# Kernel tuning notes

Hardware: AMD Instinct MI355X
Metric: run time of the kernel (lower is better)

Reference implementation:

```python
import jax, jax.numpy as jnp
import numpy as np

TOKENS = 1024
IN_W = 512
BLOCK = 256
OUT_W = 512
N_BLOCKS = 64
K = 2


def setup_inputs() -> dict:
    key = jax.random.key(0)
    ks = jax.random.split(key, 8)
    u = lambda k, s: jax.random.uniform(k, s, jnp.float32, -1.0, 1.0)
    return {
        "x": jax.random.normal(ks[0], (TOKENS, IN_W), jnp.float32),
        "noise": jax.random.normal(ks[1], (TOKENS, N_BLOCKS), jnp.float32),
        "w1s": u(ks[2], (N_BLOCKS, IN_W, BLOCK)),
        "b1s": u(ks[3], (N_BLOCKS, BLOCK)),
        "w2s": u(ks[4], (N_BLOCKS, BLOCK, OUT_W)),
        "b2s": u(ks[5], (N_BLOCKS, OUT_W)),
        "mixer": jnp.zeros((IN_W, N_BLOCKS), jnp.float32) + 0.01 * jax.random.normal(ks[6], (IN_W, N_BLOCKS), jnp.float32),
        "noise_controller": jnp.zeros((IN_W, N_BLOCKS), jnp.float32) + 0.01 * jax.random.normal(ks[7], (IN_W, N_BLOCKS), jnp.float32),
        "k": K,
    }


def reference(x, noise, w1s, b1s, w2s, b2s, mixer, noise_controller, k):
    # noisy routing logits: mixer_prod + randn * softplus(noise_prod)
    h_x = x @ mixer + noise * jax.nn.softplus(x @ noise_controller)  # [B, E]
    topk_vals, topk_idx = jax.lax.top_k(h_x, k)                       # [B, K]
    scores = jax.nn.softmax(topk_vals, axis=-1)                       # [B, K]
    # per-token expert weight gather (faithful to index_select semantics)
    gw1 = w1s[topk_idx]  # [B, K, I, H]
    gb1 = b1s[topk_idx]  # [B, K, H]
    gw2 = w2s[topk_idx]  # [B, K, H, O]
    gb2 = b2s[topk_idx]  # [B, K, O]
    v = jax.nn.relu(jnp.einsum('bi,bkih->bkh', x, gw1) + gb1)        # [B, K, H]
    out = jnp.einsum('bkh,bkho->bko', v, gw2) + gb2                   # [B, K, O]
    return jnp.sum(out * scores[..., None], axis=1)                   # [B, O]
```

## Files before the change

### kernel.cpp

```cpp
#include <hip/hip_runtime.h>
#include <math.h>

#define TOKENS    1024
#define IN_W      512
#define BLOCK_H   256
#define OUT_W     512
#define N_EXPERTS 64
#define TOPK      2
#define NSLOTS    (TOKENS * TOPK)
#define LIST_CAP  128
#define T_GRP     12
#define NGRP      4
#define XPAD      520
#define OSPAD     516
#define VPAD      264

__global__ __launch_bounds__(256) void routing_kernel(
    const float* __restrict__ x, const float* __restrict__ noise,
    const float* __restrict__ mixer, const float* __restrict__ noisec,
    float* __restrict__ esc, int* __restrict__ counts, int* __restrict__ lists)
{
    __shared__ float xs[2 * 512];
    __shared__ float pm[2 * 2 * 64];
    __shared__ float pn[2 * 2 * 64];
    const int blk  = blockIdx.x;
    const int tid  = threadIdx.x;
    const int wave = tid >> 6, lane = tid & 63;
    const int tq = wave >> 1;
    const int ih = wave & 1;

    ((float4*)xs)[tid] = ((const float4*)x)[(size_t)blk * 256 + tid];
    __syncthreads();

    float am = 0.f, an = 0.f;
    const float* xp = xs + tq * 512 + ih * 256;
    const float* mp = mixer  + (size_t)(ih * 256) * 64 + lane;
    const float* np = noisec + (size_t)(ih * 256) * 64 + lane;
    #pragma unroll 8
    for (int i = 0; i < 256; ++i) {
        const float xv = xp[i];
        am = fmaf(xv, mp[i * 64], am);
        an = fmaf(xv, np[i * 64], an);
    }
    pm[tq * 128 + ih * 64 + lane] = am;
    pn[tq * 128 + ih * 64 + lane] = an;
    __syncthreads();

    if (tid < 128) {
        const int e = tid & 63, tt = tid >> 6;
        const int t = blk * 2 + tt;
        const float am2 = pm[tt * 128 + e] + pm[tt * 128 + 64 + e];
        const float an2 = pn[tt * 128 + e] + pn[tt * 128 + 64 + e];
        const float sp = fmaxf(an2, 0.f) + log1pf(expf(-fabsf(an2)));
        pm[tt * 128 + e] = am2 + noise[(size_t)t * 64 + e] * sp;
    }
    __syncthreads();

    if (tid < 2) {
        const float* h = pm + tid * 128;
        float b0 = -INFINITY, b1 = -INFINITY;
        int i0 = 0, i1 = 0;
        for (int i = 0; i < N_EXPERTS; ++i) {
            const float v = h[i];
            if (v > b0)      { b1 = b0; i1 = i0; b0 = v; i0 = i; }
            else if (v > b1) { b1 = v; i1 = i; }
        }
        const float z   = expf(b1 - b0);
        const float inv = 1.f / (1.f + z);
        const int t = blk * 2 + tid;
        esc[t * 2 + 0] = inv;
        esc[t * 2 + 1] = z * inv;
        const int p0 = atomicAdd(&counts[i0], 1);
        if (p0 < LIST_CAP) lists[i0 * LIST_CAP + p0] = t * 2 + 0;
        const int p1 = atomicAdd(&counts[i1], 1);
        if (p1 < LIST_CAP) lists[i1 * LIST_CAP + p1] = t * 2 + 1;
    }
}

__global__ __launch_bounds__(1024, 4) void expert_kernel(
    const float* __restrict__ x,
    const float* __restrict__ w1s, const float* __restrict__ b1s,
    const float* __restrict__ w2s, const float* __restrict__ b2s,
    const int* __restrict__ counts, const int* __restrict__ lists,
    const float* __restrict__ esc, float* __restrict__ out)
{
    __shared__ __align__(16) float smem[T_GRP * XPAD];
    __shared__ __align__(16) float vsm[T_GRP * VPAD];
    __shared__ int   slotIds[T_GRP];
    __shared__ float escv[T_GRP];

    const int e  = blockIdx.x;
    const int g  = blockIdx.y;
    const int ne = min(counts[e], LIST_CAP);
    const int tid  = threadIdx.x;
    const int wave = tid >> 6, lane = tid & 63;

    const int c4 = lane & 15;
    const int r4 = (lane >> 4) << 2;
    const int cq1   = wave & 3;
    const int t0_1  = (wave >> 2) * 3;
    const int wcol1 = cq1 * 16 + c4;
    const int co2   = wave & 7;
    const int t0_2  = (wave >> 3) * 6;
    const int wcol2 = co2 * 16 + c4;

    const float4* w1v = (const float4*)(w1s + (size_t)e * IN_W * BLOCK_H);
    const float4* w2v = (const float4*)(w2s + (size_t)e * BLOCK_H * OUT_W);
    const float4* b1v = (const float4*)(b1s + (size_t)e * BLOCK_H);
    const float4* b2v = (const float4*)(b2s + (size_t)e * OUT_W);
    const float4* x4  = (const float4*)x;

    for (int base = g * T_GRP; base < ne; base += NGRP * T_GRP) {
        const int nTok = min(T_GRP, ne - base);
        if (tid < T_GRP) {
            const int s = (tid < nTok) ? lists[e * LIST_CAP + base + tid] : 0;
            slotIds[tid] = s;
            escv[tid]    = esc[s];
        }
        __syncthreads();

        for (int idx = tid; idx < T_GRP * 128; idx += 1024) {
            const int t = idx >> 7, q = idx & 127;
            float4 v = make_float4(0.f, 0.f, 0.f, 0.f);
            if (t < nTok) v = x4[(size_t)(slotIds[t] >> 1) * 128 + q];
            *(float4*)&smem[t * XPAD + q * 4] = v;
        }
        __syncthreads();

        {
            float4 a0 = make_float4(0.f,0.f,0.f,0.f), a1 = a0, a2 = a0;
            const float4* wp  = w1v + (size_t)r4 * 64 + wcol1;
            const float*  xr0 = smem + (t0_1 + 0) * XPAD + r4;
            const float*  xr1 = smem + (t0_1 + 1) * XPAD + r4;
            const float*  xr2 = smem + (t0_1 + 2) * XPAD + r4;
            float4 wb[4], wc[4];
            #pragma unroll
            for (int k = 0; k < 4; ++k) wb[k] = wp[(size_t)k * 64];
            for (int i = 0; i < IN_W; i += 16) {
                #pragma unroll
                for (int k = 0; k < 4; ++k) wc[k] = wb[k];
                if (i + 16 < IN_W) {
                    #pragma unroll
                    for (int k = 0; k < 4; ++k)
                        wb[k] = wp[(size_t)(i + 16 + k) * 64];
                }
                const float4 xv0 = *(const float4*)(xr0 + i);
                const float4 xv1 = *(const float4*)(xr1 + i);
                const float4 xv2 = *(const float4*)(xr2 + i);
                const float* f0 = (const float*)&xv0;
                const float* f1 = (const float*)&xv1;
                const float* f2 = (const float*)&xv2;
                #pragma unroll
                for (int k = 0; k < 4; ++k) {
                    const float4 w = wc[k];
                    a0.x = fmaf(f0[k], w.x, a0.x); a0.y = fmaf(f0[k], w.y, a0.y);
                    a0.z = fmaf(f0[k], w.z, a0.z); a0.w = fmaf(f0[k], w.w, a0.w);
                    a1.x = fmaf(f1[k], w.x, a1.x); a1.y = fmaf(f1[k], w.y, a1.y);
                    a1.z = fmaf(f1[k], w.z, a1.z); a1.w = fmaf(f1[k], w.w, a1.w);
                    a2.x = fmaf(f2[k], w.x, a2.x); a2.y = fmaf(f2[k], w.y, a2.y);
                    a2.z = fmaf(f2[k], w.z, a2.z); a2.w = fmaf(f2[k], w.w, a2.w);
                }
            }
            #pragma unroll
            for (int m = 16; m <= 32; m <<= 1) {
                a0.x += __shfl_xor(a0.x, m); a0.y += __shfl_xor(a0.y, m);
                a0.z += __shfl_xor(a0.z, m); a0.w += __shfl_xor(a0.w, m);
                a1.x += __shfl_xor(a1.x, m); a1.y += __shfl_xor(a1.y, m);
                a1.z += __shfl_xor(a1.z, m); a1.w += __shfl_xor(a1.w, m);
                a2.x += __shfl_xor(a2.x, m); a2.y += __shfl_xor(a2.y, m);
                a2.z += __shfl_xor(a2.z, m); a2.w += __shfl_xor(a2.w, m);
            }
            if (lane < 16) {
                const float4 bb = b1v[wcol1];
                float4 r;
                r.x = fmaxf(a0.x + bb.x, 0.f); r.y = fmaxf(a0.y + bb.y, 0.f);
                r.z = fmaxf(a0.z + bb.z, 0.f); r.w = fmaxf(a0.w + bb.w, 0.f);
                *(float4*)&vsm[(t0_1 + 0) * VPAD + wcol1 * 4] = r;
                r.x = fmaxf(a1.x + bb.x, 0.f); r.y = fmaxf(a1.y + bb.y, 0.f);
                r.z = fmaxf(a1.z + bb.z, 0.f); r.w = fmaxf(a1.w + bb.w, 0.f);
                *(float4*)&vsm[(t0_1 + 1) * VPAD + wcol1 * 4] = r;
                r.x = fmaxf(a2.x + bb.x, 0.f); r.y = fmaxf(a2.y + bb.y, 0.f);
                r.z = fmaxf(a2.z + bb.z, 0.f); r.w = fmaxf(a2.w + bb.w, 0.f);
                *(float4*)&vsm[(t0_1 + 2) * VPAD + wcol1 * 4] = r;
            }
        }
        __syncthreads();

        {
            float4 acc[6];
            #pragma unroll
            for (int j = 0; j < 6; ++j) acc[j] = make_float4(0.f,0.f,0.f,0.f);
            const float4* wp2 = w2v + (size_t)r4 * 128 + wcol2;
            const float*  vr  = vsm + t0_2 * VPAD + r4;
            float4 wb[4], wc[4];
            #pragma unroll
            for (int k = 0; k < 4; ++k) wb[k] = wp2[(size_t)k * 128];
            for (int h = 0; h < BLOCK_H; h += 16) {
                #pragma unroll
                for (int k = 0; k < 4; ++k) wc[k] = wb[k];
                if (h + 16 < BLOCK_H) {
                    #pragma unroll
                    for (int k = 0; k < 4; ++k)
                        wb[k] = wp2[(size_t)(h + 16 + k) * 128];
                }
                float4 vv[6];
                #pragma unroll
                for (int j = 0; j < 6; ++j)
                    vv[j] = *(const float4*)(vr + j * VPAD + h);
                #pragma unroll
                for (int k = 0; k < 4; ++k) {
                    const float4 w = wc[k];
                    #pragma unroll
                    for (int j = 0; j < 6; ++j) {
                        const float s = ((const float*)&vv[j])[k];
                        acc[j].x = fmaf(s, w.x, acc[j].x);
                        acc[j].y = fmaf(s, w.y, acc[j].y);
                        acc[j].z = fmaf(s, w.z, acc[j].z);
                        acc[j].w = fmaf(s, w.w, acc[j].w);
                    }
                }
            }
            #pragma unroll
            for (int m = 16; m <= 32; m <<= 1) {
                #pragma unroll
                for (int j = 0; j < 6; ++j) {
                    acc[j].x += __shfl_xor(acc[j].x, m);
                    acc[j].y += __shfl_xor(acc[j].y, m);
                    acc[j].z += __shfl_xor(acc[j].z, m);
                    acc[j].w += __shfl_xor(acc[j].w, m);
                }
            }
            if (lane < 16) {
                #pragma unroll
                for (int j = 0; j < 6; ++j)
                    *(float4*)&smem[(t0_2 + j) * OSPAD + wcol2 * 4] = acc[j];
            }
        }
        __syncthreads();

        for (int idx = tid; idx < T_GRP * 128; idx += 1024) {
            const int t = idx >> 7, q = idx & 127;
            if (t < nTok) {
                const float4 r  = *(const float4*)&smem[t * OSPAD + q * 4];
                const float4 bb = b2v[q];
                const float  sc = escv[t];
                float* o = out + (size_t)(slotIds[t] >> 1) * OUT_W + q * 4;
                atomicAdd(o + 0, (r.x + bb.x) * sc);
                atomicAdd(o + 1, (r.y + bb.y) * sc);
                atomicAdd(o + 2, (r.z + bb.z) * sc);
                atomicAdd(o + 3, (r.w + bb.w) * sc);
            }
        }
        __syncthreads();
    }
}

extern "C" void kernel_launch(void* const* d_in, const int* in_sizes, int n_in,
                              void* d_out, int out_size, void* d_ws, size_t ws_size,
                              hipStream_t stream) {
    const float* x      = (const float*)d_in[0];
    const float* noise  = (const float*)d_in[1];
    const float* w1s    = (const float*)d_in[2];
    const float* b1s    = (const float*)d_in[3];
    const float* w2s    = (const float*)d_in[4];
    const float* b2s    = (const float*)d_in[5];
    const float* mixer  = (const float*)d_in[6];
    const float* noisec = (const float*)d_in[7];
    float* out = (float*)d_out;

    char* ws = (char*)d_ws;
    int*   counts = (int*)ws;                       ws += 256;
    float* esc    = (float*)ws;                     ws += NSLOTS * sizeof(float);
    int*   lists  = (int*)ws;

    hipMemsetAsync(d_out, 0, (size_t)out_size * sizeof(float), stream);
    hipMemsetAsync(counts, 0, 256, stream);

    routing_kernel<<<TOKENS / 2, 256, 0, stream>>>(x, noise, mixer, noisec,
                                                   esc, counts, lists);
    expert_kernel<<<dim3(N_EXPERTS, NGRP), 1024, 0, stream>>>(
        x, w1s, b1s, w2s, b2s, counts, lists, esc, out);
}
```

Baseline: 185.0 us.

## Split expert GEMM reduction across waves so each weight is loaded once

Both expert matmuls are remapped so every wave covers all 12 tokens of the group for a slice of the reduction dimension. Stage 1 uses a 4-way K split and stage 2 a 2-way K split, instead of splitting tokens across waves. Before, each weight element was fetched by several waves, one per token subset. Now it is fetched once per block and reused across all tokens held in registers. Partial sums go through a new shared-memory buffer and are combined by an extra reduction pass and barrier. This costs more LDS (lower occupancy) and more accumulator registers.

Result: slower. 298.4 us (+61.3%).

```diff
diff --git a/kernel.cpp b/kernel.cpp
--- a/kernel.cpp
+++ b/kernel.cpp
@@ -12,8 +12,13 @@
 #define T_GRP     12
 #define NGRP      4
 #define XPAD      520
-#define OSPAD     516
-#define VPAD      264
+#define VPAD      260
+#define P2PAD     516
+
+__device__ __forceinline__ void fma4(float4& a, float s, const float4& w) {
+    a.x = fmaf(s, w.x, a.x); a.y = fmaf(s, w.y, a.y);
+    a.z = fmaf(s, w.z, a.z); a.w = fmaf(s, w.w, a.w);
+}
 
 __global__ __launch_bounds__(256) void routing_kernel(
     const float* __restrict__ x, const float* __restrict__ noise,
@@ -84,8 +89,9 @@
     const int* __restrict__ counts, const int* __restrict__ lists,
     const float* __restrict__ esc, float* __restrict__ out)
 {
-    __shared__ __align__(16) float smem[T_GRP * XPAD];
+    __shared__ __align__(16) float xs[T_GRP * XPAD];
     __shared__ __align__(16) float vsm[T_GRP * VPAD];
+    __shared__ __align__(16) float psum[4 * T_GRP * VPAD];
     __shared__ int   slotIds[T_GRP];
     __shared__ float escv[T_GRP];
 
@@ -94,15 +100,15 @@
     const int ne = min(counts[e], LIST_CAP);
     const int tid  = threadIdx.x;
     const int wave = tid >> 6, lane = tid & 63;
-
     const int c4 = lane & 15;
-    const int r4 = (lane >> 4) << 2;
-    const int cq1   = wave & 3;
-    const int t0_1  = (wave >> 2) * 3;
-    const int wcol1 = cq1 * 16 + c4;
-    const int co2   = wave & 7;
-    const int t0_2  = (wave >> 3) * 6;
-    const int wcol2 = co2 * 16 + c4;
+    const int rg = lane >> 4;
+
+    const int cq   = wave & 3,  kq = wave >> 2;
+    const int col1 = cq * 16 + c4;
+    const int k1   = kq * 128 + rg * 4;
+    const int oct  = wave & 7,  kh = wave >> 3;
+    const int col2 = oct * 16 + c4;
+    const int k2   = kh * 128 + rg * 4;
 
     const float4* w1v = (const float4*)(w1s + (size_t)e * IN_W * BLOCK_H);
     const float4* w2v = (const float4*)(w2s + (size_t)e * BLOCK_H * OUT_W);
@@ -123,117 +129,110 @@
             const int t = idx >> 7, q = idx & 127;
             float4 v = make_float4(0.f, 0.f, 0.f, 0.f);
             if (t < nTok) v = x4[(size_t)(slotIds[t] >> 1) * 128 + q];
-            *(float4*)&smem[t * XPAD + q * 4] = v;
+            *(float4*)&xs[t * XPAD + q * 4] = v;
         }
         __syncthreads();
 
         {
-            float4 a0 = make_float4(0.f,0.f,0.f,0.f), a1 = a0, a2 = a0;
-            const float4* wp  = w1v + (size_t)r4 * 64 + wcol1;
-            const float*  xr0 = smem + (t0_1 + 0) * XPAD + r4;
-            const float*  xr1 = smem + (t0_1 + 1) * XPAD + r4;
-            const float*  xr2 = smem + (t0_1 + 2) * XPAD + r4;
-            float4 wb[4], wc[4];
+            float4 acc[T_GRP];
+            #pragma unroll
+            for (int t = 0; t < T_GRP; ++t) acc[t] = make_float4(0.f,0.f,0.f,0.f);
+            const float4* wp = w1v + (size_t)k1 * 64 + col1;
+            float4 wb[4];
             #pragma unroll
             for (int k = 0; k < 4; ++k) wb[k] = wp[(size_t)k * 64];
-            for (int i = 0; i < IN_W; i += 16) {
+            for (int i = 0; i < 128; i += 16) {
+                float4 wc[4];
                 #pragma unroll
                 for (int k = 0; k < 4; ++k) wc[k] = wb[k];
-                if (i + 16 < IN_W) {
+                if (i + 16 < 128) {
                     #pragma unroll
                     for (int k = 0; k < 4; ++k)
                         wb[k] = wp[(size_t)(i + 16 + k) * 64];
                 }
-                const float4 xv0 = *(const float4*)(xr0 + i);
-                const float4 xv1 = *(const float4*)(xr1 + i);
-                const float4 xv2 = *(const float4*)(xr2 + i);
-                const float* f0 = (const float*)&xv0;
-                const float* f1 = (const float*)&xv1;
-                const float* f2 = (const float*)&xv2;
-                #pragma unroll
-                for (int k = 0; k < 4; ++k) {
-                    const float4 w = wc[k];
-                    a0.x = fmaf(f0[k], w.x, a0.x); a0.y = fmaf(f0[k], w.y, a0.y);
-                    a0.z = fmaf(f0[k], w.z, a0.z); a0.w = fmaf(f0[k], w.w, a0.w);
-                    a1.x = fmaf(f1[k], w.x, a1.x); a1.y = fmaf(f1[k], w.y, a1.y);
-                    a1.z = fmaf(f1[k], w.z, a1.z); a1.w = fmaf(f1[k], w.w, a1.w);
-                    a2.x = fmaf(f2[k], w.x, a2.x); a2.y = fmaf(f2[k], w.y, a2.y);
-                    a2.z = fmaf(f2[k], w.z, a2.z); a2.w = fmaf(f2[k], w.w, a2.w);
+                #pragma unroll
+                for (int t = 0; t < T_GRP; ++t) {
+                    const float4 xv = *(const float4*)&xs[t * XPAD + k1 + i];
+                    fma4(acc[t], xv.x, wc[0]);
+                    fma4(acc[t], xv.y, wc[1]);
+                    fma4(acc[t], xv.z, wc[2]);
+                    fma4(acc[t], xv.w, wc[3]);
                 }
             }
             #pragma unroll
             for (int m = 16; m <= 32; m <<= 1) {
-                a0.x += __shfl_xor(a0.x, m); a0.y += __shfl_xor(a0.y, m);
-                a0.z += __shfl_xor(a0.z, m); a0.w += __shfl_xor(a0.w, m);
-                a1.x += __shfl_xor(a1.x, m); a1.y += __shfl_xor(a1.y, m);
-                a1.z += __shfl_xor(a1.z, m); a1.w += __shfl_xor(a1.w, m);
-                a2.x += __shfl_xor(a2.x, m); a2.y += __shfl_xor(a2.y, m);
-                a2.z += __shfl_xor(a2.z, m); a2.w += __shfl_xor(a2.w, m);
+                #pragma unroll
+                for (int t = 0; t < T_GRP; ++t) {
+                    acc[t].x += __shfl_xor(acc[t].x, m);
+                    acc[t].y += __shfl_xor(acc[t].y, m);
+                    acc[t].z += __shfl_xor(acc[t].z, m);
+                    acc[t].w += __shfl_xor(acc[t].w, m);
+                }
             }
             if (lane < 16) {
-                const float4 bb = b1v[wcol1];
-                float4 r;
-                r.x = fmaxf(a0.x + bb.x, 0.f); r.y = fmaxf(a0.y + bb.y, 0.f);
-                r.z = fmaxf(a0.z + bb.z, 0.f); r.w = fmaxf(a0.w + bb.w, 0.f);
-                *(float4*)&vsm[(t0_1 + 0) * VPAD + wcol1 * 4] = r;
-                r.x = fmaxf(a1.x + bb.x, 0.f); r.y = fmaxf(a1.y + bb.y, 0.f);
-                r.z = fmaxf(a1.z + bb.z, 0.f); r.w = fmaxf(a1.w + bb.w, 0.f);
-                *(float4*)&vsm[(t0_1 + 1) * VPAD + wcol1 * 4] = r;
-                r.x = fmaxf(a2.x + bb.x, 0.f); r.y = fmaxf(a2.y + bb.y, 0.f);
-                r.z = fmaxf(a2.z + bb.z, 0.f); r.w = fmaxf(a2.w + bb.w, 0.f);
-                *(float4*)&vsm[(t0_1 + 2) * VPAD + wcol1 * 4] = r;
-            }
+                #pragma unroll
+                for (int t = 0; t < T_GRP; ++t)
+                    *(float4*)&psum[(kq * T_GRP + t) * VPAD + col1 * 4] = acc[t];
+            }
+        }
+        __syncthreads();
+
+        if (tid < T_GRP * 64) {
+            const int t = tid >> 6, c = tid & 63;
+            const float4 s0 = *(const float4*)&psum[(0 * T_GRP + t) * VPAD + c * 4];
+            const float4 s1 = *(const float4*)&psum[(1 * T_GRP + t) * VPAD + c * 4];
+            const float4 s2 = *(const float4*)&psum[(2 * T_GRP + t) * VPAD + c * 4];
+            const float4 s3 = *(const float4*)&psum[(3 * T_GRP + t) * VPAD + c * 4];
+            const float4 bb = b1v[c];
+            float4 r;
+            r.x = fmaxf(s0.x + s1.x + s2.x + s3.x + bb.x, 0.f);
+            r.y = fmaxf(s0.y + s1.y + s2.y + s3.y + bb.y, 0.f);
+            r.z = fmaxf(s0.z + s1.z + s2.z + s3.z + bb.z, 0.f);
+            r.w = fmaxf(s0.w + s1.w + s2.w + s3.w + bb.w, 0.f);
+            *(float4*)&vsm[t * VPAD + c * 4] = r;
         }
         __syncthreads();
 
         {
-            float4 acc[6];
-            #pragma unroll
-            for (int j = 0; j < 6; ++j) acc[j] = make_float4(0.f,0.f,0.f,0.f);
-            const float4* wp2 = w2v + (size_t)r4 * 128 + wcol2;
-            const float*  vr  = vsm + t0_2 * VPAD + r4;
-            float4 wb[4], wc[4];
+            float4 acc[T_GRP];
+            #pragma unroll
+            for (int t = 0; t < T_GRP; ++t) acc[t] = make_float4(0.f,0.f,0.f,0.f);
+            const float4* wp2 = w2v + (size_t)k2 * 128 + col2;
+            float4 wb[4];
             #pragma unroll
             for (int k = 0; k < 4; ++k) wb[k] = wp2[(size_t)k * 128];
-            for (int h = 0; h < BLOCK_H; h += 16) {
+            for (int i = 0; i < 128; i += 16) {
+                float4 wc[4];
                 #pragma unroll
                 for (int k = 0; k < 4; ++k) wc[k] = wb[k];
-                if (h + 16 < BLOCK_H) {
+                if (i + 16 < 128) {
                     #pragma unroll
                     for (int k = 0; k < 4; ++k)
-                        wb[k] = wp2[(size_t)(h + 16 + k) * 128];
-                }
-                float4 vv[6];
-                #pragma unroll
-                for (int j = 0; j < 6; ++j)
-                    vv[j] = *(const float4*)(vr + j * VPAD + h);
-                #pragma unroll
-                for (int k = 0; k < 4; ++k) {
-                    const float4 w = wc[k];
-                    #pragma unroll
-                    for (int j = 0; j < 6; ++j) {
-                        const float s = ((const float*)&vv[j])[k];
-                        acc[j].x = fmaf(s, w.x, acc[j].x);
-                        acc[j].y = fmaf(s, w.y, acc[j].y);
-                        acc[j].z = fmaf(s, w.z, acc[j].z);
-                        acc[j].w = fmaf(s, w.w, acc[j].w);
-                    }
+                        wb[k] = wp2[(size_t)(i + 16 + k) * 128];
+                }
+                #pragma unroll
+                for (int t = 0; t < T_GRP; ++t) {
+                    const float4 vv = *(const float4*)&vsm[t * VPAD + k2 + i];
+                    fma4(acc[t], vv.x, wc[0]);
+                    fma4(acc[t], vv.y, wc[1]);
+                    fma4(acc[t], vv.z, wc[2]);
+                    fma4(acc[t], vv.w, wc[3]);
                 }
             }
             #pragma unroll
             for (int m = 16; m <= 32; m <<= 1) {
                 #pragma unroll
-                for (int j = 0; j < 6; ++j) {
-                    acc[j].x += __shfl_xor(acc[j].x, m);
-                    acc[j].y += __shfl_xor(acc[j].y, m);
-                    acc[j].z += __shfl_xor(acc[j].z, m);
-                    acc[j].w += __shfl_xor(acc[j].w, m);
+                for (int t = 0; t < T_GRP; ++t) {
+                    acc[t].x += __shfl_xor(acc[t].x, m);
+                    acc[t].y += __shfl_xor(acc[t].y, m);
+                    acc[t].z += __shfl_xor(acc[t].z, m);
+                    acc[t].w += __shfl_xor(acc[t].w, m);
                 }
             }
             if (lane < 16) {
                 #pragma unroll
-                for (int j = 0; j < 6; ++j)
-                    *(float4*)&smem[(t0_2 + j) * OSPAD + wcol2 * 4] = acc[j];
+                for (int t = 0; t < T_GRP; ++t)
+                    *(float4*)&psum[(kh * T_GRP + t) * P2PAD + col2 * 4] = acc[t];
             }
         }
         __syncthreads();
@@ -241,14 +240,15 @@
         for (int idx = tid; idx < T_GRP * 128; idx += 1024) {
             const int t = idx >> 7, q = idx & 127;
             if (t < nTok) {
-                const float4 r  = *(const float4*)&smem[t * OSPAD + q * 4];
+                const float4 s0 = *(const float4*)&psum[(0 * T_GRP + t) * P2PAD + q * 4];
+                const float4 s1 = *(const float4*)&psum[(1 * T_GRP + t) * P2PAD + q * 4];
                 const float4 bb = b2v[q];
                 const float  sc = escv[t];
                 float* o = out + (size_t)(slotIds[t] >> 1) * OUT_W + q * 4;
-                atomicAdd(o + 0, (r.x + bb.x) * sc);
-                atomicAdd(o + 1, (r.y + bb.y) * sc);
-                atomicAdd(o + 2, (r.z + bb.z) * sc);
-                atomicAdd(o + 3, (r.w + bb.w) * sc);
+                atomicAdd(o + 0, (s0.x + s1.x + bb.x) * sc);
+                atomicAdd(o + 1, (s0.y + s1.y + bb.y) * sc);
+                atomicAdd(o + 2, (s0.z + s1.z + bb.z) * sc);
+                atomicAdd(o + 3, (s0.w + s1.w + bb.w) * sc);
             }
         }
         __syncthreads();
```
